# Performance work log

Hardware: AMD Instinct MI355X
Metric: run time of the kernel (lower is better)

The kernel has to match this reference:

```python
import math
import jax, jax.numpy as jnp
import numpy as np

C, B, T, D = 8, 4, 8192, 64
MAX_LEN = 8192
_DELTA = math.log2(MAX_LEN) / max(C - 1, 1)
# lam_c = 1 - 2^{-(c*delta)}; lam_0 == 0 (memoryless channel)
LAMBDAS = jnp.array([1.0 - 2.0 ** (-(c * _DELTA)) for c in range(C)], dtype=jnp.float32)


def setup_inputs() -> dict:
    key = jax.random.key(0)
    k0, k1, k2 = jax.random.split(key, 3)
    return {
        "channels": jax.random.normal(k0, (C, B, T, D), dtype=jnp.float32),
        "gw_fwd": jax.random.normal(k1, (C, D, D), dtype=jnp.float32) * 0.02,
        "gb_fwd": jnp.ones((C, D), dtype=jnp.float32),
        "gw_bwd": jax.random.normal(k2, (C, D, D), dtype=jnp.float32) * 0.02,
        "gb_bwd": jnp.ones((C, D), dtype=jnp.float32),
    }


def _fixed_decay_scan(lam, v):
    """h_t = lam * h_{t-1} + v_t over axis=1 (time); v: [B,T,D], lam scalar.
    For lam==0 this reduces to identity, matching the torch fast path."""
    a = jnp.full_like(v, lam)

    def combine(x, y):
        a1, b1 = x
        a2, b2 = y
        return (a1 * a2, a2 * b1 + b2)

    return jax.lax.associative_scan(combine, (a, v), axis=1)[1]


def _run_direction(channels, W, b):
    # torch Linear: y = x @ W.T + b, W is (out,in) -> einsum 'cbtd,ced->cbte'
    g = jax.nn.sigmoid(jnp.einsum('cbtd,ced->cbte', channels, W) + b[:, None, None, :])
    gated = g * channels
    return jax.vmap(_fixed_decay_scan)(LAMBDAS, gated)  # [C,B,T,D]


def reference(channels, gw_fwd, gb_fwd, gw_bwd, gb_bwd):
    fwd = _run_direction(channels, gw_fwd, gb_fwd)
    rev = channels[:, :, ::-1, :]
    bwd = _run_direction(rev, gw_bwd, gb_bwd)[:, :, ::-1, :]
    return fwd, bwd
```

## Files before the change

### kernel.cpp

```cpp
#include <hip/hip_runtime.h>
#include <cmath>
#include <cstdint>

typedef __attribute__((ext_vector_type(8))) short short8;
typedef __attribute__((ext_vector_type(4))) float f32x4;
typedef __attribute__((ext_vector_type(2))) unsigned int u32x2;

struct Lams { float v[8]; };

#define NC 8
#define NB 4
#define NT 8192
#define ND 64
#define CL 256
#define NCHUNK 32
#define NKK 16
#define NBLK (2 * NC * NB * NKK)
#define NSLOT (2 * NC * NB * NCHUNK)
#define NWAVE 8
#define LDH 72

__device__ __forceinline__ uint32_t pk2(float lo, float hi) {
    uint32_t r;
    asm("v_cvt_pk_bf16_f32 %0, %1, %2" : "=v"(r) : "v"(lo), "v"(hi));
    return r;
}

__device__ __forceinline__ float bf2f(unsigned short s) {
    return __builtin_bit_cast(float, (uint32_t)s << 16);
}

__global__ __launch_bounds__(512, 4) void k1_fused(
    const float* __restrict__ x, const float* __restrict__ Wf,
    const float* __restrict__ bf, const float* __restrict__ Wb,
    const float* __restrict__ bb, float* __restrict__ out,
    int* __restrict__ flags, float* __restrict__ evals, Lams lams)
{
    __shared__ unsigned short xbuf[CL * LDH];
    __shared__ float ends_lds[NWAVE][ND];
    __shared__ float hprev_lds[ND];

    const int tid  = threadIdx.x;
    const int lane = tid & 63;
    const int w    = tid >> 6;

    int idx = blockIdx.x;
    const int kk  = idx & (NKK - 1); idx >>= 4;
    const int b   = idx & (NB - 1);  idx >>= 2;
    const int c   = idx & (NC - 1);  idx >>= 3;
    const int dir = idx;

    const float lam = lams.v[c];
    const float* W    = (dir ? Wb : Wf) + c * ND * ND;
    const float* bias = (dir ? bb : bf) + c * ND;
    const float* xb   = x + (size_t)(c * NB + b) * NT * ND;
    float* ob = out + (size_t)dir * (size_t)(NC*NB*NT*ND)
                    + (size_t)(c * NB + b) * NT * ND;
    const int seqbase = (int)(blockIdx.x >> 4) * NCHUNK;

    const int er = lane & 15;
    const int ks = lane >> 4;
    const int r0 = w * 32;

    short8 bfrag[4][2];
    #pragma unroll
    for (int et = 0; et < 4; ++et) {
        const float* wr = W + (et*16 + er) * ND + ks * 8;
        #pragma unroll
        for (int kq = 0; kq < 2; ++kq) {
            f32x4 lo = *reinterpret_cast<const f32x4*>(wr + kq*32);
            f32x4 hi = *reinterpret_cast<const f32x4*>(wr + kq*32 + 4);
            union { short8 s8; uint32_t u[4]; } t;
            t.u[0] = pk2(lo[0], lo[1]); t.u[1] = pk2(lo[2], lo[3]);
            t.u[2] = pk2(hi[0], hi[1]); t.u[3] = pk2(hi[2], hi[3]);
            bfrag[et][kq] = t.s8;
        }
    }
    float bias_r[4];
    #pragma unroll
    for (int et = 0; et < 4; ++et) bias_r[et] = bias[et*16 + er];

    float lam32 = lam*lam; lam32*=lam32; lam32*=lam32; lam32*=lam32; lam32*=lam32;

    #pragma unroll 1
    for (int pass = 0; pass < 2; ++pass) {
        const int g   = kk + NKK * pass;
        const int tr0 = g * CL;

        {
            const int sr = lane >> 4;
            const int sc = (lane & 15) * 4;
            if (dir == 0) {
                const float* p = xb + (size_t)(tr0 + r0 + sr) * ND + sc;
                #pragma unroll
                for (int q = 0; q < 8; ++q) {
                    f32x4 v = *reinterpret_cast<const f32x4*>(p + (size_t)q * 4 * ND);
                    u32x2 u = { pk2(v[0], v[1]), pk2(v[2], v[3]) };
                    *reinterpret_cast<u32x2*>(&xbuf[(r0 + q*4 + sr) * LDH + sc]) = u;
                }
            } else {
                const float* p = xb + (size_t)(NT-1 - (tr0 + r0 + sr)) * ND + sc;
                #pragma unroll
                for (int q = 0; q < 8; ++q) {
                    f32x4 v = *reinterpret_cast<const f32x4*>(p - (size_t)q * 4 * ND);
                    u32x2 u = { pk2(v[0], v[1]), pk2(v[2], v[3]) };
                    *reinterpret_cast<u32x2*>(&xbuf[(r0 + q*4 + sr) * LDH + sc]) = u;
                }
            }
        }

        #pragma unroll
        for (int u = 0; u < 2; ++u) {
            const int rl0 = r0 + u*16;
            short8 afrag[2];
            afrag[0] = *reinterpret_cast<const short8*>(&xbuf[(rl0 + er) * LDH + ks * 8]);
            afrag[1] = *reinterpret_cast<const short8*>(&xbuf[(rl0 + er) * LDH + 32 + ks * 8]);
            #pragma unroll
            for (int et = 0; et < 4; ++et) {
                f32x4 acc = {0.f, 0.f, 0.f, 0.f};
                acc = __builtin_amdgcn_mfma_f32_16x16x32_bf16(afrag[0], bfrag[et][0], acc, 0,0,0);
                acc = __builtin_amdgcn_mfma_f32_16x16x32_bf16(afrag[1], bfrag[et][1], acc, 0,0,0);
                const int col = et*16 + er;
                float gated[4];
                #pragma unroll
                for (int r = 0; r < 4; ++r) {
                    const int rl = rl0 + ks*4 + r;
                    float z  = acc[r] + bias_r[et];
                    float gg = __builtin_amdgcn_rcpf(1.0f + __expf(-z));
                    float xv = bf2f(xbuf[rl * LDH + col]);
                    gated[r] = gg * xv;
                }
                uint32_t p01 = pk2(gated[0], gated[1]);
                uint32_t p23 = pk2(gated[2], gated[3]);
                xbuf[(rl0 + ks*4 + 0) * LDH + col] = (unsigned short)(p01 & 0xFFFF);
                xbuf[(rl0 + ks*4 + 1) * LDH + col] = (unsigned short)(p01 >> 16);
                xbuf[(rl0 + ks*4 + 2) * LDH + col] = (unsigned short)(p23 & 0xFFFF);
                xbuf[(rl0 + ks*4 + 3) * LDH + col] = (unsigned short)(p23 >> 16);
            }
        }

        {
            float h = 0.f;
            #pragma unroll
            for (int i = 0; i < 32; ++i) {
                const int a = (r0 + i) * LDH + lane;
                float v = bf2f(xbuf[a]);
                h = fmaf(h, lam, v);
                xbuf[a] = (unsigned short)(pk2(h, h) & 0xFFFF);
            }
            ends_lds[w][lane] = h;
        }
        __syncthreads();

        if (w == NWAVE - 1) {
            float carryW = 0.f;
            #pragma unroll
            for (int j = 0; j < NWAVE - 1; ++j)
                carryW = fmaf(carryW, lam32, ends_lds[j][lane]);
            float E = fmaf(carryW, lam32, ends_lds[NWAVE-1][lane]);

            float Hprev = 0.f;
            if (c != 0) {
                const int slot = seqbase + g;
                __hip_atomic_store(&evals[(size_t)slot * ND + lane], E,
                                   __ATOMIC_RELAXED, __HIP_MEMORY_SCOPE_AGENT);
                asm volatile("s_waitcnt vmcnt(0)" ::: "memory");
                if (lane == 0)
                    __hip_atomic_store(&flags[slot], 1, __ATOMIC_RELAXED,
                                       __HIP_MEMORY_SCOPE_AGENT);
                if (g != 0) {
                    if (lane < g) {
                        while (__hip_atomic_load(&flags[seqbase + lane], __ATOMIC_RELAXED,
                                                 __HIP_MEMORY_SCOPE_AGENT) == 0)
                            __builtin_amdgcn_s_sleep(8);
                    }
                    asm volatile("" ::: "memory");
                    const float* eb = evals + (size_t)seqbase * ND;
                    float l1 = lam32*lam32; l1 *= l1; l1 *= l1;
                    float l4 = l1 * l1; l4 *= l4;
                    float P = 0.f;
                    int j = 0;
                    const int rem = g & 3;
                    for (; j < rem; ++j)
                        P = fmaf(P, l1, eb[(size_t)j * ND + lane]);
                    for (; j < g; j += 4) {
                        float e0 = eb[(size_t)(j+0) * ND + lane];
                        float e1 = eb[(size_t)(j+1) * ND + lane];
                        float e2 = eb[(size_t)(j+2) * ND + lane];
                        float e3 = eb[(size_t)(j+3) * ND + lane];
                        float t = fmaf(fmaf(fmaf(e0, l1, e1), l1, e2), l1, e3);
                        P = fmaf(P, l4, t);
                    }
                    Hprev = P;
                }
            }
            hprev_lds[lane] = Hprev;
        }
        __syncthreads();

        {
            const int sr = lane >> 4;
            const int dg = lane & 15;
            float carry4[4];
            #pragma unroll
            for (int j2 = 0; j2 < 4; ++j2) {
                const int d = dg*4 + j2;
                float cy = 0.f, pw = 1.f;
                for (int j = 0; j < w; ++j) {
                    cy = fmaf(cy, lam32, ends_lds[j][d]);
                    pw *= lam32;
                }
                carry4[j2] = fmaf(pw, hprev_lds[d], cy);
            }
            const float lam2 = lam * lam, lam4 = lam2 * lam2;
            float f = lam;
            for (int j = 0; j < sr; ++j) f *= lam;
            if (dir == 0) {
                float* p = ob + (size_t)(tr0 + r0 + sr) * ND + dg*4;
                #pragma unroll
                for (int q = 0; q < 8; ++q) {
                    u32x2 hv = *reinterpret_cast<const u32x2*>(
                        &xbuf[(r0 + q*4 + sr) * LDH + dg*4]);
                    f32x4 o;
                    o[0] = fmaf(f, carry4[0], bf2f((unsigned short)(hv[0] & 0xFFFF)));
                    o[1] = fmaf(f, carry4[1], bf2f((unsigned short)(hv[0] >> 16)));
                    o[2] = fmaf(f, carry4[2], bf2f((unsigned short)(hv[1] & 0xFFFF)));
                    o[3] = fmaf(f, carry4[3], bf2f((unsigned short)(hv[1] >> 16)));
                    *reinterpret_cast<f32x4*>(p + (size_t)q * 4 * ND) = o;
                    f *= lam4;
                }
            } else {
                float* p = ob + (size_t)(NT-1 - (tr0 + r0 + sr)) * ND + dg*4;
                #pragma unroll
                for (int q = 0; q < 8; ++q) {
                    u32x2 hv = *reinterpret_cast<const u32x2*>(
                        &xbuf[(r0 + q*4 + sr) * LDH + dg*4]);
                    f32x4 o;
                    o[0] = fmaf(f, carry4[0], bf2f((unsigned short)(hv[0] & 0xFFFF)));
                    o[1] = fmaf(f, carry4[1], bf2f((unsigned short)(hv[0] >> 16)));
                    o[2] = fmaf(f, carry4[2], bf2f((unsigned short)(hv[1] & 0xFFFF)));
                    o[3] = fmaf(f, carry4[3], bf2f((unsigned short)(hv[1] >> 16)));
                    *reinterpret_cast<f32x4*>(p - (size_t)q * 4 * ND) = o;
                    f *= lam4;
                }
            }
        }
        __syncthreads();
    }
}

extern "C" void kernel_launch(void* const* d_in, const int* in_sizes, int n_in,
                              void* d_out, int out_size, void* d_ws, size_t ws_size,
                              hipStream_t stream)
{
    const float* x  = (const float*)d_in[0];
    const float* Wf = (const float*)d_in[1];
    const float* bf = (const float*)d_in[2];
    const float* Wb = (const float*)d_in[3];
    const float* bb = (const float*)d_in[4];
    float* out = (float*)d_out;

    int*   flags = (int*)d_ws;
    float* evals = (float*)((char*)d_ws + 16384);

    Lams lams;
    const double delta = 13.0 / 7.0;
    for (int c = 0; c < 8; ++c)
        lams.v[c] = (float)(1.0 - pow(2.0, -(double)c * delta));

    hipMemsetAsync(flags, 0, NSLOT * 4, stream);

    dim3 grid(NBLK);
    k1_fused<<<grid, 512, 0, stream>>>(x, Wf, bf, Wb, bb, out, flags, evals, lams);
}
```

Measured before the change: 70.77 us.

## Store gated values transposed in LDS and load MFMA A-fragments from global

Replaces the row-major bf16 LDS tile with a transposed, channel-major u32 buffer. Each lane now owns one feature column, so the sequential scan and the output pass use 128-bit LDS accesses instead of scalar 16-bit ones. The MFMA A-fragments are now read directly from global memory and converted, rather than read back from LDS. The cost is per-lane strided scalar global loads and stores (one float per row), a second global read of x for the GEMM, and extra barriers between stages.

```diff
diff --git a/kernel.cpp b/kernel.cpp
--- a/kernel.cpp
+++ b/kernel.cpp
@@ -5,6 +5,7 @@
 typedef __attribute__((ext_vector_type(8))) short short8;
 typedef __attribute__((ext_vector_type(4))) float f32x4;
 typedef __attribute__((ext_vector_type(2))) unsigned int u32x2;
+typedef __attribute__((ext_vector_type(4))) unsigned int u32x4;
 
 struct Lams { float v[8]; };
 
@@ -18,7 +19,7 @@
 #define NBLK (2 * NC * NB * NKK)
 #define NSLOT (2 * NC * NB * NCHUNK)
 #define NWAVE 8
-#define LDH 72
+#define TR32 132
 
 __device__ __forceinline__ uint32_t pk2(float lo, float hi) {
     uint32_t r;
@@ -28,6 +29,15 @@
 
 __device__ __forceinline__ float bf2f(unsigned short s) {
     return __builtin_bit_cast(float, (uint32_t)s << 16);
+}
+__device__ __forceinline__ float bflo(uint32_t u) { return bf2f((unsigned short)(u & 0xFFFFu)); }
+__device__ __forceinline__ float bfhi(uint32_t u) { return bf2f((unsigned short)(u >> 16)); }
+
+__device__ __forceinline__ short8 cvt8(f32x4 a, f32x4 b) {
+    union { short8 s8; uint32_t u[4]; } t;
+    t.u[0] = pk2(a[0], a[1]); t.u[1] = pk2(a[2], a[3]);
+    t.u[2] = pk2(b[0], b[1]); t.u[3] = pk2(b[2], b[3]);
+    return t.s8;
 }
 
 __global__ __launch_bounds__(512, 4) void k1_fused(
@@ -36,7 +46,7 @@
     const float* __restrict__ bb, float* __restrict__ out,
     int* __restrict__ flags, float* __restrict__ evals, Lams lams)
 {
-    __shared__ unsigned short xbuf[CL * LDH];
+    __shared__ uint32_t tbuf[ND * TR32];
     __shared__ float ends_lds[NWAVE][ND];
     __shared__ float hprev_lds[ND];
 
@@ -70,10 +80,7 @@
         for (int kq = 0; kq < 2; ++kq) {
             f32x4 lo = *reinterpret_cast<const f32x4*>(wr + kq*32);
             f32x4 hi = *reinterpret_cast<const f32x4*>(wr + kq*32 + 4);
-            union { short8 s8; uint32_t u[4]; } t;
-            t.u[0] = pk2(lo[0], lo[1]); t.u[1] = pk2(lo[2], lo[3]);
-            t.u[2] = pk2(hi[0], hi[1]); t.u[3] = pk2(hi[2], hi[3]);
-            bfrag[et][kq] = t.s8;
+            bfrag[et][kq] = cvt8(lo, hi);
         }
     }
     float bias_r[4];
@@ -88,65 +95,75 @@
         const int tr0 = g * CL;
 
         {
-            const int sr = lane >> 4;
-            const int sc = (lane & 15) * 4;
-            if (dir == 0) {
-                const float* p = xb + (size_t)(tr0 + r0 + sr) * ND + sc;
-                #pragma unroll
-                for (int q = 0; q < 8; ++q) {
-                    f32x4 v = *reinterpret_cast<const f32x4*>(p + (size_t)q * 4 * ND);
-                    u32x2 u = { pk2(v[0], v[1]), pk2(v[2], v[3]) };
-                    *reinterpret_cast<u32x2*>(&xbuf[(r0 + q*4 + sr) * LDH + sc]) = u;
-                }
-            } else {
-                const float* p = xb + (size_t)(NT-1 - (tr0 + r0 + sr)) * ND + sc;
-                #pragma unroll
-                for (int q = 0; q < 8; ++q) {
-                    f32x4 v = *reinterpret_cast<const f32x4*>(p - (size_t)q * 4 * ND);
-                    u32x2 u = { pk2(v[0], v[1]), pk2(v[2], v[3]) };
-                    *reinterpret_cast<u32x2*>(&xbuf[(r0 + q*4 + sr) * LDH + sc]) = u;
-                }
-            }
-        }
+            const float* sp = dir
+                ? xb + (size_t)(NT-1 - (tr0 + r0)) * ND + lane
+                : xb + (size_t)(tr0 + r0) * ND + lane;
+            const ptrdiff_t step = dir ? -(ptrdiff_t)ND : (ptrdiff_t)ND;
+            #pragma unroll
+            for (int q = 0; q < 4; ++q) {
+                float v[8];
+                #pragma unroll
+                for (int i = 0; i < 8; ++i)
+                    v[i] = sp[(ptrdiff_t)(q*8 + i) * step];
+                u32x4 pk = { pk2(v[0], v[1]), pk2(v[2], v[3]),
+                             pk2(v[4], v[5]), pk2(v[6], v[7]) };
+                *reinterpret_cast<u32x4*>(&tbuf[lane * TR32 + 16*w + 4*q]) = pk;
+            }
+        }
+        __syncthreads();
 
         #pragma unroll
         for (int u = 0; u < 2; ++u) {
-            const int rl0 = r0 + u*16;
+            const int trow = tr0 + r0 + u*16;
             short8 afrag[2];
-            afrag[0] = *reinterpret_cast<const short8*>(&xbuf[(rl0 + er) * LDH + ks * 8]);
-            afrag[1] = *reinterpret_cast<const short8*>(&xbuf[(rl0 + er) * LDH + 32 + ks * 8]);
+            {
+                const int tg = dir ? (NT-1 - (trow + er)) : (trow + er);
+                const float* xr = xb + (size_t)tg * ND + ks * 8;
+                #pragma unroll
+                for (int kq = 0; kq < 2; ++kq) {
+                    f32x4 lo = *reinterpret_cast<const f32x4*>(xr + kq*32);
+                    f32x4 hi = *reinterpret_cast<const f32x4*>(xr + kq*32 + 4);
+                    afrag[kq] = cvt8(lo, hi);
+                }
+            }
             #pragma unroll
             for (int et = 0; et < 4; ++et) {
                 f32x4 acc = {0.f, 0.f, 0.f, 0.f};
                 acc = __builtin_amdgcn_mfma_f32_16x16x32_bf16(afrag[0], bfrag[et][0], acc, 0,0,0);
                 acc = __builtin_amdgcn_mfma_f32_16x16x32_bf16(afrag[1], bfrag[et][1], acc, 0,0,0);
                 const int col = et*16 + er;
+                uint32_t* tb = &tbuf[col * TR32 + 16*w + 8*u + 2*ks];
+                u32x2 xv2 = *reinterpret_cast<const u32x2*>(tb);
+                float xv[4] = { bflo(xv2[0]), bfhi(xv2[0]),
+                                bflo(xv2[1]), bfhi(xv2[1]) };
                 float gated[4];
                 #pragma unroll
                 for (int r = 0; r < 4; ++r) {
-                    const int rl = rl0 + ks*4 + r;
                     float z  = acc[r] + bias_r[et];
                     float gg = __builtin_amdgcn_rcpf(1.0f + __expf(-z));
-                    float xv = bf2f(xbuf[rl * LDH + col]);
-                    gated[r] = gg * xv;
-                }
-                uint32_t p01 = pk2(gated[0], gated[1]);
-                uint32_t p23 = pk2(gated[2], gated[3]);
-                xbuf[(rl0 + ks*4 + 0) * LDH + col] = (unsigned short)(p01 & 0xFFFF);
-                xbuf[(rl0 + ks*4 + 1) * LDH + col] = (unsigned short)(p01 >> 16);
-                xbuf[(rl0 + ks*4 + 2) * LDH + col] = (unsigned short)(p23 & 0xFFFF);
-                xbuf[(rl0 + ks*4 + 3) * LDH + col] = (unsigned short)(p23 >> 16);
-            }
-        }
+                    gated[r] = gg * xv[r];
+                }
+                u32x2 gp = { pk2(gated[0], gated[1]), pk2(gated[2], gated[3]) };
+                *reinterpret_cast<u32x2*>(tb) = gp;
+            }
+        }
+        __syncthreads();
 
         {
             float h = 0.f;
-            #pragma unroll
-            for (int i = 0; i < 32; ++i) {
-                const int a = (r0 + i) * LDH + lane;
-                float v = bf2f(xbuf[a]);
-                h = fmaf(h, lam, v);
-                xbuf[a] = (unsigned short)(pk2(h, h) & 0xFFFF);
+            uint32_t* tc = &tbuf[lane * TR32 + 16*w];
+            #pragma unroll
+            for (int q = 0; q < 4; ++q) {
+                u32x4 vv = *reinterpret_cast<const u32x4*>(&tc[4*q]);
+                u32x4 hh;
+                #pragma unroll
+                for (int j = 0; j < 4; ++j) {
+                    float h0 = fmaf(h, lam, bflo(vv[j]));
+                    float h1 = fmaf(h0, lam, bfhi(vv[j]));
+                    hh[j] = pk2(h0, h1);
+                    h = h1;
+                }
+                *reinterpret_cast<u32x4*>(&tc[4*q]) = hh;
             }
             ends_lds[w][lane] = h;
         }
@@ -199,49 +216,28 @@
         __syncthreads();
 
         {
-            const int sr = lane >> 4;
-            const int dg = lane & 15;
-            float carry4[4];
-            #pragma unroll
-            for (int j2 = 0; j2 < 4; ++j2) {
-                const int d = dg*4 + j2;
-                float cy = 0.f, pw = 1.f;
-                for (int j = 0; j < w; ++j) {
-                    cy = fmaf(cy, lam32, ends_lds[j][d]);
-                    pw *= lam32;
-                }
-                carry4[j2] = fmaf(pw, hprev_lds[d], cy);
-            }
-            const float lam2 = lam * lam, lam4 = lam2 * lam2;
+            float cy = 0.f, pw = 1.f;
+            for (int j = 0; j < w; ++j) {
+                cy = fmaf(cy, lam32, ends_lds[j][lane]);
+                pw *= lam32;
+            }
+            const float carry = fmaf(pw, hprev_lds[lane], cy);
+
+            float* p = dir
+                ? ob + (size_t)(NT-1 - (tr0 + r0)) * ND + lane
+                : ob + (size_t)(tr0 + r0) * ND + lane;
+            const ptrdiff_t step = dir ? -(ptrdiff_t)ND : (ptrdiff_t)ND;
+            const uint32_t* tc = &tbuf[lane * TR32 + 16*w];
             float f = lam;
-            for (int j = 0; j < sr; ++j) f *= lam;
-            if (dir == 0) {
-                float* p = ob + (size_t)(tr0 + r0 + sr) * ND + dg*4;
-                #pragma unroll
-                for (int q = 0; q < 8; ++q) {
-                    u32x2 hv = *reinterpret_cast<const u32x2*>(
-                        &xbuf[(r0 + q*4 + sr) * LDH + dg*4]);
-                    f32x4 o;
-                    o[0] = fmaf(f, carry4[0], bf2f((unsigned short)(hv[0] & 0xFFFF)));
-                    o[1] = fmaf(f, carry4[1], bf2f((unsigned short)(hv[0] >> 16)));
-                    o[2] = fmaf(f, carry4[2], bf2f((unsigned short)(hv[1] & 0xFFFF)));
-                    o[3] = fmaf(f, carry4[3], bf2f((unsigned short)(hv[1] >> 16)));
-                    *reinterpret_cast<f32x4*>(p + (size_t)q * 4 * ND) = o;
-                    f *= lam4;
-                }
-            } else {
-                float* p = ob + (size_t)(NT-1 - (tr0 + r0 + sr)) * ND + dg*4;
-                #pragma unroll
-                for (int q = 0; q < 8; ++q) {
-                    u32x2 hv = *reinterpret_cast<const u32x2*>(
-                        &xbuf[(r0 + q*4 + sr) * LDH + dg*4]);
-                    f32x4 o;
-                    o[0] = fmaf(f, carry4[0], bf2f((unsigned short)(hv[0] & 0xFFFF)));
-                    o[1] = fmaf(f, carry4[1], bf2f((unsigned short)(hv[0] >> 16)));
-                    o[2] = fmaf(f, carry4[2], bf2f((unsigned short)(hv[1] & 0xFFFF)));
-                    o[3] = fmaf(f, carry4[3], bf2f((unsigned short)(hv[1] >> 16)));
-                    *reinterpret_cast<f32x4*>(p - (size_t)q * 4 * ND) = o;
-                    f *= lam4;
+            #pragma unroll
+            for (int q = 0; q < 4; ++q) {
+                u32x4 vv = *reinterpret_cast<const u32x4*>(&tc[4*q]);
+                #pragma unroll
+                for (int j = 0; j < 4; ++j) {
+                    p[(ptrdiff_t)(q*8 + 2*j) * step]     = fmaf(f, carry, bflo(vv[j]));
+                    f *= lam;
+                    p[(ptrdiff_t)(q*8 + 2*j + 1) * step] = fmaf(f, carry, bfhi(vv[j]));
+                    f *= lam;
                 }
             }
         }
```

Measured after the change: 99.10 us. +40.0%, slower.
